# Performance work log

Hardware: AMD Instinct MI355X
Metric: run time of the kernel (lower is better)

Reference implementation:

```python
import jax, jax.numpy as jnp
import numpy as np

EMB = 256   # EMB_SIZE hard-coded in source
H = 8       # num heads (all heads share the same Q/K/V, as in source)
DK = EMB // H  # 32
B, T = 16, 2048
LN_EPS = 1e-5


def _layernorm(a, g, b):
    m = jnp.mean(a, axis=-1, keepdims=True)
    v = jnp.mean(jnp.square(a - m), axis=-1, keepdims=True)
    return (a - m) * jax.lax.rsqrt(v + LN_EPS) * g + b


def setup_inputs() -> dict:
    key = jax.random.key(0)
    ks = jax.random.split(key, 8)
    sc = 0.02
    return {
        "x": jax.random.normal(ks[0], (B, T, EMB), jnp.float32),
        "Wq": jax.random.normal(ks[1], (EMB, DK), jnp.float32) * sc,
        "Wk": jax.random.normal(ks[2], (EMB, DK), jnp.float32) * sc,
        "Wv": jax.random.normal(ks[3], (EMB, DK), jnp.float32) * sc,
        "Wp": jax.random.normal(ks[4], (EMB, EMB), jnp.float32) * sc,
        "bp": jnp.zeros((EMB,), jnp.float32),
        "W1": jax.random.normal(ks[5], (EMB, 4 * EMB), jnp.float32) * sc,
        "b1": jnp.zeros((4 * EMB,), jnp.float32),
        "W2": jax.random.normal(ks[6], (4 * EMB, EMB), jnp.float32) * sc,
        "b2": jnp.zeros((EMB,), jnp.float32),
        "g1": jnp.ones((EMB,), jnp.float32),
        "be1": jnp.zeros((EMB,), jnp.float32),
        "g2": jnp.ones((EMB,), jnp.float32),
        "be2": jnp.zeros((EMB,), jnp.float32),
    }


def reference(x, Wq, Wk, Wv, Wp, bp, W1, b1, W2, b2, g1, be1, g2, be2):
    # Single shared-head QKV projections (bias-free), as in source
    q = x @ Wq  # [B,T,DK]
    k = x @ Wk
    v = x @ Wv
    # Causal self-attention with explicit score matrix [B,T,T]
    scores = jnp.einsum("btd,bsd->bts", q, k) / jnp.sqrt(jnp.float32(DK))
    causal = jnp.tril(jnp.ones((T, T), dtype=bool))
    scores = jnp.where(causal, scores, -jnp.inf)
    a = jax.nn.softmax(scores, axis=-1)
    attn = jnp.einsum("bts,bsd->btd", a, v)  # [B,T,DK]
    # Source concatenates h identical copies of the same attention output
    cat = jnp.tile(attn, (1, 1, H))  # [B,T,EMB]
    mh = cat @ Wp + bp
    y1 = _layernorm(x + mh, g1, be1)
    ff = jax.nn.gelu(y1 @ W1 + b1, approximate=False) @ W2 + b2
    return _layernorm(y1 + ff, g2, be2)
```

## Files before the change

### kernel.cpp

```cpp
#include <hip/hip_runtime.h>

#define BB 16
#define TT 2048
#define EE 256
#define DK 32
#define MM (BB*TT)
#define FF 1024

typedef __bf16 bf16_t;
typedef __bf16 bf16x8 __attribute__((ext_vector_type(8)));
typedef __bf16 bf16x4 __attribute__((ext_vector_type(4)));
typedef float  f32x4  __attribute__((ext_vector_type(4)));

__device__ __forceinline__ f32x4 mfma16(bf16x8 a, bf16x8 b, f32x4 c){
  return __builtin_amdgcn_mfma_f32_16x16x32_bf16(a, b, c, 0, 0, 0);
}
__device__ __forceinline__ void gload_lds16(const void* g, void* l){
  __builtin_amdgcn_global_load_lds((__attribute__((address_space(1))) void*)g,
                                   (__attribute__((address_space(3))) void*)l,
                                   16, 0, 0);
}

__launch_bounds__(256)
__global__ void prep_kernel(const float* __restrict__ Wq, const float* __restrict__ Wk,
                            const float* __restrict__ Wv, const float* __restrict__ Wp,
                            const float* __restrict__ W1, const float* __restrict__ W2,
                            bf16_t* __restrict__ wqkv, float* __restrict__ wpe,
                            bf16_t* __restrict__ w1t, bf16_t* __restrict__ w2t)
{
  const int i = blockIdx.x*256 + threadIdx.x;
  if (i < 96*256) {
    const int r = i >> 8, c = i & 255;
    float v;
    if (r < 32)      v = Wq[c*32 + r] * 0.17677669529663687f;
    else if (r < 64) v = Wk[c*32 + (r-32)];
    else             v = Wv[c*32 + (r-64)];
    wqkv[i] = (bf16_t)v;
  }
  if (i < 32*256) {
    const int d = i >> 8, n = i & 255;
    float s = 0.f;
    #pragma unroll
    for (int h = 0; h < 8; ++h) s += Wp[(h*32 + d)*256 + n];
    wpe[i] = s;
  }
  if (i < 1024*256) {
    const int n = i >> 8, k = i & 255;
    w1t[i] = (bf16_t)W1[(size_t)k*1024 + n];
  }
  if (i < 256*1024) {
    const int n = i >> 10, k = i & 1023;
    w2t[i] = (bf16_t)W2[(size_t)k*256 + n];
  }
}

__launch_bounds__(256)
__global__ void qkv_kernel(const float* __restrict__ x, const bf16_t* __restrict__ wqkv,
                           bf16_t* __restrict__ q, bf16_t* __restrict__ kd,
                           bf16_t* __restrict__ vT)
{
  __shared__ bf16_t Ws[96*256];
  bf16_t* Vt = Ws;
  const int tid = threadIdx.x;
  #pragma unroll
  for (int i = 0; i < 12; ++i) {
    const int v8  = tid + i*256;
    const int row = v8 >> 5;
    const int bir = (v8 & 31) * 16;
    *(bf16x8*)((char*)Ws + row*512 + (bir ^ ((row & 7) << 4))) =
        *(const bf16x8*)(wqkv + (size_t)v8*8);
  }
  __syncthreads();

  const int w = tid >> 6, l = tid & 63;
  const int lr = l & 15, lk4 = l >> 4, lkb = lk4*8;
  const int m0 = blockIdx.x * 64;
  const int arow = m0 + w*16 + lr;
  const float* xr = x + (size_t)arow * 256;

  f32x4 acc[6] = {};
  #pragma unroll
  for (int s = 0; s < 8; ++s) {
    const int kb = s*32 + lkb;
    const float4 v0 = *(const float4*)(xr + kb);
    const float4 v1 = *(const float4*)(xr + kb + 4);
    bf16x8 a;
    a[0]=(bf16_t)v0.x; a[1]=(bf16_t)v0.y; a[2]=(bf16_t)v0.z; a[3]=(bf16_t)v0.w;
    a[4]=(bf16_t)v1.x; a[5]=(bf16_t)v1.y; a[6]=(bf16_t)v1.z; a[7]=(bf16_t)v1.w;
    #pragma unroll
    for (int j = 0; j < 6; ++j) {
      const int nrow = j*16 + lr;
      const bf16x8 bf = *(const bf16x8*)((const char*)Ws + nrow*512 +
                                         ((kb*2) ^ ((nrow & 7) << 4)));
      acc[j] = mfma16(a, bf, acc[j]);
    }
  }
  #pragma unroll
  for (int j = 0; j < 4; ++j) {
    #pragma unroll
    for (int r = 0; r < 4; ++r) {
      const int orow = m0 + w*16 + lk4*4 + r;
      const int col  = j*16 + lr;
      const bf16_t v = (bf16_t)acc[j][r];
      if (col < 32) q[(size_t)orow*32 + col] = v;
      else          kd[(size_t)orow*32 + (col-32)] = v;
    }
  }
  __syncthreads();
  #pragma unroll
  for (int j = 4; j < 6; ++j)
    #pragma unroll
    for (int r = 0; r < 4; ++r) {
      const int d = (j-4)*16 + lr;
      const int t = w*16 + lk4*4 + r;
      *(bf16_t*)((char*)Vt + d*128 + ((((t>>3) ^ (d&7))<<4) | ((t&7)*2))) =
          (bf16_t)acc[j][r];
    }
  __syncthreads();
  {
    const int d = tid >> 3, c8 = tid & 7;
    const bf16x8 v = *(const bf16x8*)((char*)Vt + d*128 + ((c8 ^ (d&7))<<4));
    *(bf16x8*)(vT + ((size_t)(m0 >> 11)*32 + d)*TT + (m0 & 2047) + c8*8) = v;
  }
}

__launch_bounds__(256)
__global__ void attnp_kernel(const bf16_t* __restrict__ q, const bf16_t* __restrict__ kd,
                             const bf16_t* __restrict__ vT,
                             float* __restrict__ part_acc, float* __restrict__ part_ml)
{
  __shared__ bf16_t P[4][16*128];
  const int tid = threadIdx.x;
  const int w = tid >> 6, l = tid & 63;
  const int wv = blockIdx.x*4 + w;
  const int lr = l & 15, g4 = l >> 4;
  const float NEG_INF = -__builtin_inff();

  const int b = wv / 320;
  const int u = wv - b*320;
  int r, base;
  if      (u >= 192) { r = 3; base = 192; }
  else if (u >= 96)  { r = 2; base = 96;  }
  else if (u >= 32)  { r = 1; base = 32;  }
  else               { r = 0; base = 0;   }
  const int qq = u - base;
  const int g  = r*32 + qq / (r+1);
  const int c  = qq - (qq / (r+1))*(r+1);
  const int t_total = (g >> 3) + 1;
  const int t0 = c*4;
  const int t1 = min(t0 + 4, t_total);

  const bf16_t* qb = q  + (size_t)b*TT*32;
  const bf16_t* kb = kd + (size_t)b*TT*32;
  const bf16_t* vb = vT + (size_t)b*32*TT;
  const int q0 = g*16;
  const int qg = q0 + lr;

  const bf16x8 qa = *(const bf16x8*)(qb + (size_t)(q0 + lr)*32 + g4*8);
  const bf16_t* v0r = vb + (size_t)lr*TT;
  const bf16_t* v1r = vb + (size_t)(16 + lr)*TT;

  f32x4 acc0 = {0.f,0.f,0.f,0.f}, acc1 = {0.f,0.f,0.f,0.f};
  float mrun = NEG_INF, lsum = 0.f;
  char* pb = (char*)&P[w][0];
  const int swz = (lr & 7) << 4;
  const f32x4 zf = {0.f,0.f,0.f,0.f};

  for (int t = t0; t < t1; ++t) {
    const int k0 = t * 128;
    f32x4 s[8];
    #pragma unroll
    for (int cc = 0; cc < 8; ++cc) {
      const bf16x8 kf = *(const bf16x8*)(kb + (size_t)(k0 + cc*16 + lr)*32 + g4*8);
      s[cc] = mfma16(kf, qa, zf);
    }
    if (t == t_total - 1) {
      #pragma unroll
      for (int cc = 0; cc < 8; ++cc)
        #pragma unroll
        for (int rr = 0; rr < 4; ++rr)
          if (k0 + cc*16 + g4*4 + rr > qg) s[cc][rr] = NEG_INF;
    }
    float mt = NEG_INF;
    #pragma unroll
    for (int cc = 0; cc < 8; ++cc) {
      float a01 = fmaxf(s[cc][0], s[cc][1]), a23 = fmaxf(s[cc][2], s[cc][3]);
      mt = fmaxf(mt, fmaxf(a01, a23));
    }
    mt = fmaxf(mt, __shfl_xor(mt, 16));
    mt = fmaxf(mt, __shfl_xor(mt, 32));
    const float mn = fmaxf(mrun, mt);
    const float sc = __expf(mrun - mn);
    float ps = 0.f;
    #pragma unroll
    for (int cc = 0; cc < 8; ++cc) {
      float p0 = __expf(s[cc][0]-mn), p1 = __expf(s[cc][1]-mn);
      float p2 = __expf(s[cc][2]-mn), p3 = __expf(s[cc][3]-mn);
      s[cc][0]=p0; s[cc][1]=p1; s[cc][2]=p2; s[cc][3]=p3;
      ps += (p0+p1) + (p2+p3);
    }
    ps += __shfl_xor(ps, 16);
    ps += __shfl_xor(ps, 32);
    lsum = lsum*sc + ps;
    mrun = mn;
    acc0 *= sc; acc1 *= sc;
    #pragma unroll
    for (int cc = 0; cc < 8; ++cc) {
      bf16x4 pk;
      pk[0]=(bf16_t)s[cc][0]; pk[1]=(bf16_t)s[cc][1];
      pk[2]=(bf16_t)s[cc][2]; pk[3]=(bf16_t)s[cc][3];
      *(bf16x4*)(pb + lr*256 + ((cc*32 + g4*8) ^ swz)) = pk;
    }
    #pragma unroll
    for (int h = 0; h < 4; ++h) {
      const bf16x8 pbf = *(const bf16x8*)(pb + lr*256 + ((h*64 + g4*16) ^ swz));
      acc0 = mfma16(*(const bf16x8*)(v0r + k0 + h*32 + g4*8), pbf, acc0);
      acc1 = mfma16(*(const bf16x8*)(v1r + k0 + h*32 + g4*8), pbf, acc1);
    }
  }
  float* pa = part_acc + (size_t)wv*512;
  *(f32x4*)(pa + l*8)     = acc0;
  *(f32x4*)(pa + l*8 + 4) = acc1;
  if (l < 16) {
    part_ml[wv*32 + l]      = mrun;
    part_ml[wv*32 + 16 + l] = lsum;
  }
}

__launch_bounds__(256)
__global__ void attnc_kernel(const float* __restrict__ part_acc,
                             const float* __restrict__ part_ml,
                             bf16_t* __restrict__ attn)
{
  const int tid = threadIdx.x;
  const int id = blockIdx.x*4 + (tid >> 6);
  const int l = tid & 63, lr = l & 15, g4 = l >> 4;
  const int b = id >> 7, g = id & 127;
  const int r = g >> 5;
  const int base = (r == 0) ? 0 : (r == 1) ? 32 : (r == 2) ? 96 : 192;
  const int p0 = b*320 + base + (g - (r << 5))*(r + 1);
  const int nc = r + 1;
  const float NEG_INF = -__builtin_inff();

  float m0v=NEG_INF,m1v=NEG_INF,m2v=NEG_INF,m3v=NEG_INF;
  float l0v=0,l1v=0,l2v=0,l3v=0;
  f32x4 a00={0,0,0,0},a01={0,0,0,0},a10={0,0,0,0},a11={0,0,0,0};
  f32x4 a20={0,0,0,0},a21={0,0,0,0},a30={0,0,0,0},a31={0,0,0,0};
  {
    const float* pa = part_acc + (size_t)p0*512;
    a00 = *(const f32x4*)(pa + l*8); a01 = *(const f32x4*)(pa + l*8 + 4);
    m0v = part_ml[p0*32 + lr]; l0v = part_ml[p0*32 + 16 + lr];
  }
  if (nc > 1) {
    const float* pa = part_acc + (size_t)(p0+1)*512;
    a10 = *(const f32x4*)(pa + l*8); a11 = *(const f32x4*)(pa + l*8 + 4);
    m1v = part_ml[(p0+1)*32 + lr]; l1v = part_ml[(p0+1)*32 + 16 + lr];
  }
  if (nc > 2) {
    const float* pa = part_acc + (size_t)(p0+2)*512;
    a20 = *(const f32x4*)(pa + l*8); a21 = *(const f32x4*)(pa + l*8 + 4);
    m2v = part_ml[(p0+2)*32 + lr]; l2v = part_ml[(p0+2)*32 + 16 + lr];
  }
  if (nc > 3) {
    const float* pa = part_acc + (size_t)(p0+3)*512;
    a30 = *(const f32x4*)(pa + l*8); a31 = *(const f32x4*)(pa + l*8 + 4);
    m3v = part_ml[(p0+3)*32 + lr]; l3v = part_ml[(p0+3)*32 + 16 + lr];
  }
  const float M = fmaxf(fmaxf(m0v, m1v), fmaxf(m2v, m3v));
  const float w0 = __expf(m0v - M), w1 = __expf(m1v - M);
  const float w2 = __expf(m2v - M), w3 = __expf(m3v - M);
  const float L = l0v*w0 + l1v*w1 + l2v*w2 + l3v*w3;
  const float inv = 1.0f / L;
  f32x4 o0 = (a00*w0 + a10*w1 + a20*w2 + a30*w3) * inv;
  f32x4 o1 = (a01*w0 + a11*w1 + a21*w2 + a31*w3) * inv;

  bf16_t* ao = attn + ((size_t)b*TT + g*16 + lr)*32;
  bf16x4 ob0, ob1;
  ob0[0]=(bf16_t)o0[0]; ob0[1]=(bf16_t)o0[1]; ob0[2]=(bf16_t)o0[2]; ob0[3]=(bf16_t)o0[3];
  ob1[0]=(bf16_t)o1[0]; ob1[1]=(bf16_t)o1[1]; ob1[2]=(bf16_t)o1[2]; ob1[3]=(bf16_t)o1[3];
  *(bf16x4*)(ao + g4*4)      = ob0;
  *(bf16x4*)(ao + 16 + g4*4) = ob1;
}

__launch_bounds__(256)
__global__ void ln1_kernel(const float* __restrict__ x, const bf16_t* __restrict__ attn,
                           const float* __restrict__ wpe, const float* __restrict__ bp,
                           const float* __restrict__ g1, const float* __restrict__ be1,
                           bf16_t* __restrict__ y1b)
{
  __shared__ float Wp_s[32*256];
  const int tid = threadIdx.x;
  for (int i = tid; i < 32*64; i += 256)
    ((float4*)Wp_s)[i] = ((const float4*)wpe)[i];
  __syncthreads();

  const int w = tid >> 6, l = tid & 63;
  const int n = l * 4;
  const float4 gv  = *(const float4*)(g1  + n);
  const float4 bev = *(const float4*)(be1 + n);
  const float4 bpv = *(const float4*)(bp  + n);

  #pragma unroll 1
  for (int it = 0; it < 8; ++it) {
    const int row = blockIdx.x*32 + it*4 + w;
    const bf16_t* ar = attn + (size_t)row*32;
    float a[32];
    #pragma unroll
    for (int i = 0; i < 4; ++i) {
      const bf16x8 t = *(const bf16x8*)(ar + i*8);
      #pragma unroll
      for (int j = 0; j < 8; ++j) a[i*8 + j] = (float)t[j];
    }
    float mh[4] = {bpv.x, bpv.y, bpv.z, bpv.w};
    #pragma unroll
    for (int d = 0; d < 32; ++d) {
      const float4 wv = *(const float4*)(Wp_s + d*256 + n);
      const float ad = a[d];
      mh[0] = fmaf(ad, wv.x, mh[0]); mh[1] = fmaf(ad, wv.y, mh[1]);
      mh[2] = fmaf(ad, wv.z, mh[2]); mh[3] = fmaf(ad, wv.w, mh[3]);
    }
    const float4 xv = *(const float4*)(x + (size_t)row*256 + n);
    const float t0 = xv.x + mh[0], t1 = xv.y + mh[1];
    const float t2 = xv.z + mh[2], t3 = xv.w + mh[3];
    float s1 = (t0+t1) + (t2+t3);
    float s2 = (t0*t0 + t1*t1) + (t2*t2 + t3*t3);
    #pragma unroll
    for (int m = 1; m < 64; m <<= 1) { s1 += __shfl_xor(s1, m); s2 += __shfl_xor(s2, m); }
    const float mean = s1 * (1.0f/256.0f);
    const float var  = s2 * (1.0f/256.0f) - mean*mean;
    const float rs   = rsqrtf(var + 1e-5f);
    float4 yv;
    yv.x = (t0-mean)*rs*gv.x + bev.x; yv.y = (t1-mean)*rs*gv.y + bev.y;
    yv.z = (t2-mean)*rs*gv.z + bev.z; yv.w = (t3-mean)*rs*gv.w + bev.w;
    bf16x4 yb; yb[0]=(bf16_t)yv.x; yb[1]=(bf16_t)yv.y; yb[2]=(bf16_t)yv.z; yb[3]=(bf16_t)yv.w;
    *(bf16x4*)(y1b + (size_t)row*256 + n) = yb;
  }
}

__launch_bounds__(512)
__global__ void mlp_kernel(const bf16_t* __restrict__ y1b, const bf16_t* __restrict__ w1t,
                           const float* __restrict__ b1, const bf16_t* __restrict__ w2t,
                           const float* __restrict__ b2, const float* __restrict__ g2,
                           const float* __restrict__ be2, float* __restrict__ out)
{
  __shared__ char SM[151552];
  const int tid = threadIdx.x;
  const int w = tid >> 6, l = tid & 63;
  const int lr = l & 15, lk4 = l >> 4;
  const int m0 = blockIdx.x * 128;
  const int wm1 = (w>>1)*32, wn1 = (w&1)*32;
  const int wm2 = (w>>2)*64, wn2 = (w&3)*64;

  {
    const float2 bv = *(const float2*)(b1 + tid*2);
    *(float2*)(SM + 147456 + tid*8) = bv;
  }
  asm volatile("s_waitcnt vmcnt(0) lgkmcnt(0)" ::: "memory");
  __builtin_amdgcn_sched_barrier(0);

  #define ST_W1(i, d)                                                         \
    { _Pragma("unroll")                                                       \
      for (int p_ = 0; p_ < 4; ++p_) {                                        \
        const int idx_ = p_*512 + tid;                                        \
        const int r_ = idx_ >> 5, c_ = idx_ & 31;                             \
        const int sc_ = (c_ & 24) | ((c_ ^ r_) & 7);                          \
        gload_lds16(w1t + (size_t)((i)*64 + r_)*256 + sc_*8,                  \
                    SM + (d)*32768 + idx_*16);                                \
      } }
  #define ST_W2(i, d)                                                         \
    { _Pragma("unroll")                                                       \
      for (int p_ = 0; p_ < 4; ++p_) {                                        \
        const int idx_ = p_*512 + tid;                                        \
        const int r_ = idx_ >> 3, c_ = idx_ & 7;                              \
        gload_lds16(w2t + (size_t)r_*1024 + (i)*64 + ((c_ ^ r_) & 7)*8,       \
                    SM + 65536 + (d)*32768 + idx_*16);                        \
      } }

  ST_W1(0, 0);
  __builtin_amdgcn_sched_barrier(0);
  bf16x8 aA[2][8];
  #pragma unroll
  for (int i2 = 0; i2 < 2; ++i2)
    #pragma unroll
    for (int kk = 0; kk < 8; ++kk)
      aA[i2][kk] = *(const bf16x8*)(y1b +
          (size_t)(m0 + wm1 + i2*16 + lr)*256 + kk*32 + lk4*8);
  __builtin_amdgcn_sched_barrier(0);
  ST_W2(0, 0);
  __builtin_amdgcn_sched_barrier(0);
  ST_W1(1, 1);
  __builtin_amdgcn_sched_barrier(0);

  f32x4 oacc[4][4] = {};

  #pragma unroll 1
  for (int i = 0; i < 16; ++i) {
    if (i < 15) { asm volatile("s_waitcnt vmcnt(8)" ::: "memory"); }
    else        { asm volatile("s_waitcnt vmcnt(4)" ::: "memory"); }
    __builtin_amdgcn_sched_barrier(0);
    __builtin_amdgcn_s_barrier();
    __builtin_amdgcn_sched_barrier(0);
    const char* sw1 = SM + (i & 1)*32768;
    f32x4 ah[2][2] = {};
    __builtin_amdgcn_s_setprio(1);
    #pragma unroll
    for (int kk = 0; kk < 8; ++kk) {
      const int off = kk*64 + lk4*16;
      const int n0r = wn1 + lr, n1r = wn1 + 16 + lr;
      const bf16x8 bf0 = *(const bf16x8*)(sw1 + n0r*512 + (off ^ ((n0r&7)<<4)));
      const bf16x8 bf1 = *(const bf16x8*)(sw1 + n1r*512 + (off ^ ((n1r&7)<<4)));
      ah[0][0] = mfma16(aA[0][kk], bf0, ah[0][0]);
      ah[0][1] = mfma16(aA[0][kk], bf1, ah[0][1]);
      ah[1][0] = mfma16(aA[1][kk], bf0, ah[1][0]);
      ah[1][1] = mfma16(aA[1][kk], bf1, ah[1][1]);
    }
    __builtin_amdgcn_s_setprio(0);
    #pragma unroll
    for (int j = 0; j < 2; ++j) {
      const float bias = *(const float*)(SM + 147456 + (i*64 + wn1 + j*16 + lr)*4);
      #pragma unroll
      for (int i2 = 0; i2 < 2; ++i2)
        #pragma unroll
        for (int r = 0; r < 4; ++r) {
          const int hrow = wm1 + i2*16 + lk4*4 + r;
          const int hcol = wn1 + j*16 + lr;
          const float v = ah[i2][j][r] + bias;
          const float z = 1.5957691216057308f * v * fmaf(0.044715f, v*v, 1.0f);
          const float gg = v * __builtin_amdgcn_rcpf(1.0f + __expf(-z));
          *(bf16_t*)(SM + 131072 + hrow*128 + ((hcol*2) ^ ((hrow&7)<<4))) = (bf16_t)gg;
        }
    }
    asm volatile("s_waitcnt lgkmcnt(0)" ::: "memory");
    __builtin_amdgcn_sched_barrier(0);
    if (i < 15) { asm volatile("s_waitcnt vmcnt(4)" ::: "memory"); }
    else        { asm volatile("s_waitcnt vmcnt(0)" ::: "memory"); }
    __builtin_amdgcn_sched_barrier(0);
    __builtin_amdgcn_s_barrier();
    __builtin_amdgcn_sched_barrier(0);
    const char* sw2 = SM + 65536 + (i & 1)*32768;
    __builtin_amdgcn_s_setprio(1);
    #pragma unroll
    for (int kk2 = 0; kk2 < 2; ++kk2) {
      const int off = kk2*64 + lk4*16;
      bf16x8 ha[4], wb[4];
      #pragma unroll
      for (int i3 = 0; i3 < 4; ++i3) {
        const int row = wm2 + i3*16 + lr;
        ha[i3] = *(const bf16x8*)(SM + 131072 + row*128 + (off ^ ((row&7)<<4)));
      }
      #pragma unroll
      for (int j3 = 0; j3 < 4; ++j3) {
        const int n = wn2 + j3*16 + lr;
        wb[j3] = *(const bf16x8*)(sw2 + n*128 + (off ^ ((n&7)<<4)));
      }
      #pragma unroll
      for (int i3 = 0; i3 < 4; ++i3)
        #pragma unroll
        for (int j3 = 0; j3 < 4; ++j3)
          oacc[i3][j3] = mfma16(ha[i3], wb[j3], oacc[i3][j3]);
    }
    __builtin_amdgcn_s_setprio(0);
    __builtin_amdgcn_sched_barrier(0);
    if (i < 15) { ST_W2(i+1, (i+1)&1); }
    __builtin_amdgcn_sched_barrier(0);
    if (i < 14) { ST_W1(i+2, i&1); }
    __builtin_amdgcn_sched_barrier(0);
  }
  #undef ST_W1
  #undef ST_W2

  float b2r[4], g2r[4], be2r[4];
  #pragma unroll
  for (int j3 = 0; j3 < 4; ++j3) {
    const int col = wn2 + j3*16 + lr;
    b2r[j3] = b2[col]; g2r[j3] = g2[col]; be2r[j3] = be2[col];
  }
  #pragma unroll
  for (int i3 = 0; i3 < 4; ++i3)
    #pragma unroll
    for (int r = 0; r < 4; ++r) {
      const int grow = m0 + wm2 + i3*16 + lk4*4 + r;
      #pragma unroll
      for (int j3 = 0; j3 < 4; ++j3) {
        const int col = wn2 + j3*16 + lr;
        oacc[i3][j3][r] += b2r[j3] + (float)y1b[(size_t)grow*256 + col];
      }
    }
  __syncthreads();
  float* red = (float*)SM;
  #pragma unroll
  for (int i3 = 0; i3 < 4; ++i3)
    #pragma unroll
    for (int r = 0; r < 4; ++r) {
      float s1 = (oacc[i3][0][r] + oacc[i3][1][r]) + (oacc[i3][2][r] + oacc[i3][3][r]);
      float s2 = (oacc[i3][0][r]*oacc[i3][0][r] + oacc[i3][1][r]*oacc[i3][1][r]) +
                 (oacc[i3][2][r]*oacc[i3][2][r] + oacc[i3][3][r]*oacc[i3][3][r]);
      #pragma unroll
      for (int m = 1; m < 16; m <<= 1) { s1 += __shfl_xor(s1, m); s2 += __shfl_xor(s2, m); }
      if (lr == 0) {
        const int rl = wm2 + i3*16 + lk4*4 + r;
        red[rl*8 + (w & 3)*2]     = s1;
        red[rl*8 + (w & 3)*2 + 1] = s2;
      }
    }
  __syncthreads();
  #pragma unroll
  for (int i3 = 0; i3 < 4; ++i3)
    #pragma unroll
    for (int r = 0; r < 4; ++r) {
      const int rl = wm2 + i3*16 + lk4*4 + r;
      const float S1 = (red[rl*8+0] + red[rl*8+2]) + (red[rl*8+4] + red[rl*8+6]);
      const float S2 = (red[rl*8+1] + red[rl*8+3]) + (red[rl*8+5] + red[rl*8+7]);
      const float mean = S1 * (1.0f/256.0f);
      const float var  = S2 * (1.0f/256.0f) - mean*mean;
      const float rs   = rsqrtf(var + 1e-5f);
      #pragma unroll
      for (int j3 = 0; j3 < 4; ++j3) {
        const int col = wn2 + j3*16 + lr;
        out[(size_t)(m0 + rl)*256 + col] = (oacc[i3][j3][r] - mean)*rs*g2r[j3] + be2r[j3];
      }
    }
}

extern "C" void kernel_launch(void* const* d_in, const int* in_sizes, int n_in,
                              void* d_out, int out_size, void* d_ws, size_t ws_size,
                              hipStream_t stream)
{
  const float* x   = (const float*)d_in[0];
  const float* Wq  = (const float*)d_in[1];
  const float* Wk  = (const float*)d_in[2];
  const float* Wv  = (const float*)d_in[3];
  const float* Wp  = (const float*)d_in[4];
  const float* bp  = (const float*)d_in[5];
  const float* W1  = (const float*)d_in[6];
  const float* b1  = (const float*)d_in[7];
  const float* W2  = (const float*)d_in[8];
  const float* b2  = (const float*)d_in[9];
  const float* g1  = (const float*)d_in[10];
  const float* be1 = (const float*)d_in[11];
  const float* g2  = (const float*)d_in[12];
  const float* be2 = (const float*)d_in[13];

  char* ws = (char*)d_ws;
  bf16_t* qd   = (bf16_t*)(ws + ((size_t)0  << 20));
  bf16_t* kd   = (bf16_t*)(ws + ((size_t)2  << 20));
  bf16_t* vTd  = (bf16_t*)(ws + ((size_t)4  << 20));
  bf16_t* attn = (bf16_t*)(ws + ((size_t)6  << 20));
  bf16_t* y1b  = (bf16_t*)(ws + ((size_t)8  << 20));
  bf16_t* wqkv = (bf16_t*)(ws + ((size_t)24 << 20));
  float*  wpe  = (float*) (ws + ((size_t)25 << 20));
  bf16_t* w1t  = (bf16_t*)(ws + ((size_t)26 << 20));
  bf16_t* w2t  = (bf16_t*)(ws + ((size_t)27 << 20));
  float*  pml  = (float*) (ws + ((size_t)28 << 20));
  float*  pacc = (float*) (ws + ((size_t)29 << 20));
  float* out = (float*)d_out;

  prep_kernel<<<1024, 256, 0, stream>>>(Wq, Wk, Wv, Wp, W1, W2, wqkv, wpe, w1t, w2t);
  qkv_kernel<<<512, 256, 0, stream>>>(x, wqkv, qd, kd, vTd);
  attnp_kernel<<<1280, 256, 0, stream>>>(qd, kd, vTd, pacc, pml);
  attnc_kernel<<<512, 256, 0, stream>>>(pacc, pml, attn);
  ln1_kernel<<<1024, 256, 0, stream>>>(x, attn, wpe, bp, g1, be1, y1b);
  mlp_kernel<<<256, 512, 0, stream>>>(y1b, w1t, b1, w2t, b2, g2, be2, out);
}
```

Baseline: 129.7 us.

## Double MLP block to 1024 threads with per-wave 16-row tiles

The fused MLP kernel now launches 16 waves per block instead of 8, and each wave owns a 16-row by 32-col slice of the hidden GEMM and a 16-row by 128-col slice of the output GEMM. Cooperative weight staging and the LayerNorm reduction are re-indexed for the wider block, with fewer loads per thread and matching vmcnt waits. Some sched_barrier fences are removed. The aim is more latency hiding per CU for the same LDS footprint, at the cost of less register-level reuse per MFMA, more LDS reads per flop, and a tighter register budget per thread.

```diff
diff --git a/kernel.cpp b/kernel.cpp
--- a/kernel.cpp
+++ b/kernel.cpp
@@ -337,7 +337,7 @@
   }
 }
 
-__launch_bounds__(512)
+__launch_bounds__(1024)
 __global__ void mlp_kernel(const bf16_t* __restrict__ y1b, const bf16_t* __restrict__ w1t,
                            const float* __restrict__ b1, const bf16_t* __restrict__ w2t,
                            const float* __restrict__ b2, const float* __restrict__ g2,
@@ -346,22 +346,20 @@
   __shared__ char SM[151552];
   const int tid = threadIdx.x;
   const int w = tid >> 6, l = tid & 63;
-  const int lr = l & 15, lk4 = l >> 4;
+  const int lr = l & 15, g4 = l >> 4;
   const int m0 = blockIdx.x * 128;
-  const int wm1 = (w>>1)*32, wn1 = (w&1)*32;
-  const int wm2 = (w>>2)*64, wn2 = (w&3)*64;
-
-  {
-    const float2 bv = *(const float2*)(b1 + tid*2);
-    *(float2*)(SM + 147456 + tid*8) = bv;
-  }
+  const int wm  = (w >> 1) * 16;
+  const int wn1 = (w & 1) * 32;
+  const int wn2 = (w & 1) * 128;
+
+  *(float*)(SM + 147456 + tid*4) = b1[tid];
   asm volatile("s_waitcnt vmcnt(0) lgkmcnt(0)" ::: "memory");
   __builtin_amdgcn_sched_barrier(0);
 
   #define ST_W1(i, d)                                                         \
     { _Pragma("unroll")                                                       \
-      for (int p_ = 0; p_ < 4; ++p_) {                                        \
-        const int idx_ = p_*512 + tid;                                        \
+      for (int p_ = 0; p_ < 2; ++p_) {                                        \
+        const int idx_ = p_*1024 + tid;                                       \
         const int r_ = idx_ >> 5, c_ = idx_ & 31;                             \
         const int sc_ = (c_ & 24) | ((c_ ^ r_) & 7);                          \
         gload_lds16(w1t + (size_t)((i)*64 + r_)*256 + sc_*8,                  \
@@ -369,157 +367,129 @@
       } }
   #define ST_W2(i, d)                                                         \
     { _Pragma("unroll")                                                       \
-      for (int p_ = 0; p_ < 4; ++p_) {                                        \
-        const int idx_ = p_*512 + tid;                                        \
+      for (int p_ = 0; p_ < 2; ++p_) {                                        \
+        const int idx_ = p_*1024 + tid;                                       \
         const int r_ = idx_ >> 3, c_ = idx_ & 7;                              \
         gload_lds16(w2t + (size_t)r_*1024 + (i)*64 + ((c_ ^ r_) & 7)*8,       \
                     SM + 65536 + (d)*32768 + idx_*16);                        \
       } }
 
   ST_W1(0, 0);
-  __builtin_amdgcn_sched_barrier(0);
-  bf16x8 aA[2][8];
-  #pragma unroll
-  for (int i2 = 0; i2 < 2; ++i2)
-    #pragma unroll
-    for (int kk = 0; kk < 8; ++kk)
-      aA[i2][kk] = *(const bf16x8*)(y1b +
-          (size_t)(m0 + wm1 + i2*16 + lr)*256 + kk*32 + lk4*8);
-  __builtin_amdgcn_sched_barrier(0);
+  bf16x8 aA[8];
+  #pragma unroll
+  for (int kk = 0; kk < 8; ++kk)
+    aA[kk] = *(const bf16x8*)(y1b + (size_t)(m0 + wm + lr)*256 + kk*32 + g4*8);
   ST_W2(0, 0);
-  __builtin_amdgcn_sched_barrier(0);
   ST_W1(1, 1);
-  __builtin_amdgcn_sched_barrier(0);
-
-  f32x4 oacc[4][4] = {};
+
+  f32x4 oacc[8] = {};
+  char* hb = SM + 131072;
 
   #pragma unroll 1
   for (int i = 0; i < 16; ++i) {
-    if (i < 15) { asm volatile("s_waitcnt vmcnt(8)" ::: "memory"); }
-    else        { asm volatile("s_waitcnt vmcnt(4)" ::: "memory"); }
+    if (i < 15) { asm volatile("s_waitcnt vmcnt(4)" ::: "memory"); }
+    else        { asm volatile("s_waitcnt vmcnt(2)" ::: "memory"); }
     __builtin_amdgcn_sched_barrier(0);
     __builtin_amdgcn_s_barrier();
-    __builtin_amdgcn_sched_barrier(0);
     const char* sw1 = SM + (i & 1)*32768;
-    f32x4 ah[2][2] = {};
+    f32x4 ah0 = {0.f,0.f,0.f,0.f}, ah1 = {0.f,0.f,0.f,0.f};
     __builtin_amdgcn_s_setprio(1);
     #pragma unroll
     for (int kk = 0; kk < 8; ++kk) {
-      const int off = kk*64 + lk4*16;
+      const int off = kk*64 + g4*16;
       const int n0r = wn1 + lr, n1r = wn1 + 16 + lr;
-      const bf16x8 bf0 = *(const bf16x8*)(sw1 + n0r*512 + (off ^ ((n0r&7)<<4)));
-      const bf16x8 bf1 = *(const bf16x8*)(sw1 + n1r*512 + (off ^ ((n1r&7)<<4)));
-      ah[0][0] = mfma16(aA[0][kk], bf0, ah[0][0]);
-      ah[0][1] = mfma16(aA[0][kk], bf1, ah[0][1]);
-      ah[1][0] = mfma16(aA[1][kk], bf0, ah[1][0]);
-      ah[1][1] = mfma16(aA[1][kk], bf1, ah[1][1]);
+      const bf16x8 bf0 = *(const bf16x8*)(sw1 + n0r*512 + (off ^ ((n0r & 7) << 4)));
+      const bf16x8 bf1 = *(const bf16x8*)(sw1 + n1r*512 + (off ^ ((n1r & 7) << 4)));
+      ah0 = mfma16(aA[kk], bf0, ah0);
+      ah1 = mfma16(aA[kk], bf1, ah1);
     }
     __builtin_amdgcn_s_setprio(0);
     #pragma unroll
     for (int j = 0; j < 2; ++j) {
       const float bias = *(const float*)(SM + 147456 + (i*64 + wn1 + j*16 + lr)*4);
+      const f32x4 av = j ? ah1 : ah0;
+      const int hcol2 = (wn1 + j*16 + lr)*2;
       #pragma unroll
-      for (int i2 = 0; i2 < 2; ++i2)
-        #pragma unroll
-        for (int r = 0; r < 4; ++r) {
-          const int hrow = wm1 + i2*16 + lk4*4 + r;
-          const int hcol = wn1 + j*16 + lr;
-          const float v = ah[i2][j][r] + bias;
-          const float z = 1.5957691216057308f * v * fmaf(0.044715f, v*v, 1.0f);
-          const float gg = v * __builtin_amdgcn_rcpf(1.0f + __expf(-z));
-          *(bf16_t*)(SM + 131072 + hrow*128 + ((hcol*2) ^ ((hrow&7)<<4))) = (bf16_t)gg;
-        }
+      for (int r = 0; r < 4; ++r) {
+        const int hrow = wm + g4*4 + r;
+        const float v = av[r] + bias;
+        const float z = 1.5957691216057308f * v * fmaf(0.044715f, v*v, 1.0f);
+        const float gg = v * __builtin_amdgcn_rcpf(1.0f + __expf(-z));
+        *(bf16_t*)(hb + hrow*128 + (hcol2 ^ ((hrow & 7) << 4))) = (bf16_t)gg;
+      }
     }
     asm volatile("s_waitcnt lgkmcnt(0)" ::: "memory");
     __builtin_amdgcn_sched_barrier(0);
-    if (i < 15) { asm volatile("s_waitcnt vmcnt(4)" ::: "memory"); }
+    if (i < 15) { asm volatile("s_waitcnt vmcnt(2)" ::: "memory"); }
     else        { asm volatile("s_waitcnt vmcnt(0)" ::: "memory"); }
     __builtin_amdgcn_sched_barrier(0);
     __builtin_amdgcn_s_barrier();
-    __builtin_amdgcn_sched_barrier(0);
     const char* sw2 = SM + 65536 + (i & 1)*32768;
     __builtin_amdgcn_s_setprio(1);
     #pragma unroll
     for (int kk2 = 0; kk2 < 2; ++kk2) {
-      const int off = kk2*64 + lk4*16;
-      bf16x8 ha[4], wb[4];
+      const int off = kk2*64 + g4*16;
+      const int hr = wm + lr;
+      const bf16x8 ha = *(const bf16x8*)(hb + hr*128 + (off ^ ((hr & 7) << 4)));
       #pragma unroll
-      for (int i3 = 0; i3 < 4; ++i3) {
-        const int row = wm2 + i3*16 + lr;
-        ha[i3] = *(const bf16x8*)(SM + 131072 + row*128 + (off ^ ((row&7)<<4)));
+      for (int j3 = 0; j3 < 8; ++j3) {
+        const int n = wn2 + j3*16 + lr;
+        const bf16x8 wb = *(const bf16x8*)(sw2 + n*128 + (off ^ ((n & 7) << 4)));
+        oacc[j3] = mfma16(ha, wb, oacc[j3]);
       }
-      #pragma unroll
-      for (int j3 = 0; j3 < 4; ++j3) {
-        const int n = wn2 + j3*16 + lr;
-        wb[j3] = *(const bf16x8*)(sw2 + n*128 + (off ^ ((n&7)<<4)));
-      }
-      #pragma unroll
-      for (int i3 = 0; i3 < 4; ++i3)
-        #pragma unroll
-        for (int j3 = 0; j3 < 4; ++j3)
-          oacc[i3][j3] = mfma16(ha[i3], wb[j3], oacc[i3][j3]);
     }
     __builtin_amdgcn_s_setprio(0);
-    __builtin_amdgcn_sched_barrier(0);
-    if (i < 15) { ST_W2(i+1, (i+1)&1); }
-    __builtin_amdgcn_sched_barrier(0);
-    if (i < 14) { ST_W1(i+2, i&1); }
-    __builtin_amdgcn_sched_barrier(0);
+    if (i < 15) ST_W2(i+1, (i+1)&1);
+    if (i < 14) ST_W1(i+2, i&1);
   }
   #undef ST_W1
   #undef ST_W2
 
-  float b2r[4], g2r[4], be2r[4];
-  #pragma unroll
-  for (int j3 = 0; j3 < 4; ++j3) {
+  float b2r[8], g2r[8], be2r[8];
+  #pragma unroll
+  for (int j3 = 0; j3 < 8; ++j3) {
     const int col = wn2 + j3*16 + lr;
     b2r[j3] = b2[col]; g2r[j3] = g2[col]; be2r[j3] = be2[col];
   }
   #pragma unroll
-  for (int i3 = 0; i3 < 4; ++i3)
-    #pragma unroll
-    for (int r = 0; r < 4; ++r) {
-      const int grow = m0 + wm2 + i3*16 + lk4*4 + r;
-      #pragma unroll
-      for (int j3 = 0; j3 < 4; ++j3) {
-        const int col = wn2 + j3*16 + lr;
-        oacc[i3][j3][r] += b2r[j3] + (float)y1b[(size_t)grow*256 + col];
-      }
-    }
+  for (int r = 0; r < 4; ++r) {
+    const int grow = m0 + wm + g4*4 + r;
+    #pragma unroll
+    for (int j3 = 0; j3 < 8; ++j3) {
+      const int col = wn2 + j3*16 + lr;
+      oacc[j3][r] += b2r[j3] + (float)y1b[(size_t)grow*256 + col];
+    }
+  }
   __syncthreads();
   float* red = (float*)SM;
   #pragma unroll
-  for (int i3 = 0; i3 < 4; ++i3)
-    #pragma unroll
-    for (int r = 0; r < 4; ++r) {
-      float s1 = (oacc[i3][0][r] + oacc[i3][1][r]) + (oacc[i3][2][r] + oacc[i3][3][r]);
-      float s2 = (oacc[i3][0][r]*oacc[i3][0][r] + oacc[i3][1][r]*oacc[i3][1][r]) +
-                 (oacc[i3][2][r]*oacc[i3][2][r] + oacc[i3][3][r]*oacc[i3][3][r]);
-      #pragma unroll
-      for (int m = 1; m < 16; m <<= 1) { s1 += __shfl_xor(s1, m); s2 += __shfl_xor(s2, m); }
-      if (lr == 0) {
-        const int rl = wm2 + i3*16 + lk4*4 + r;
-        red[rl*8 + (w & 3)*2]     = s1;
-        red[rl*8 + (w & 3)*2 + 1] = s2;
-      }
-    }
+  for (int r = 0; r < 4; ++r) {
+    float s1 = 0.f, s2 = 0.f;
+    #pragma unroll
+    for (int j3 = 0; j3 < 8; ++j3) { s1 += oacc[j3][r]; s2 += oacc[j3][r]*oacc[j3][r]; }
+    #pragma unroll
+    for (int m = 1; m < 16; m <<= 1) { s1 += __shfl_xor(s1, m); s2 += __shfl_xor(s2, m); }
+    if (lr == 0) {
+      const int rl = wm + g4*4 + r;
+      red[rl*4 + (w & 1)*2]     = s1;
+      red[rl*4 + (w & 1)*2 + 1] = s2;
+    }
+  }
   __syncthreads();
   #pragma unroll
-  for (int i3 = 0; i3 < 4; ++i3)
-    #pragma unroll
-    for (int r = 0; r < 4; ++r) {
-      const int rl = wm2 + i3*16 + lk4*4 + r;
-      const float S1 = (red[rl*8+0] + red[rl*8+2]) + (red[rl*8+4] + red[rl*8+6]);
-      const float S2 = (red[rl*8+1] + red[rl*8+3]) + (red[rl*8+5] + red[rl*8+7]);
-      const float mean = S1 * (1.0f/256.0f);
-      const float var  = S2 * (1.0f/256.0f) - mean*mean;
-      const float rs   = rsqrtf(var + 1e-5f);
-      #pragma unroll
-      for (int j3 = 0; j3 < 4; ++j3) {
-        const int col = wn2 + j3*16 + lr;
-        out[(size_t)(m0 + rl)*256 + col] = (oacc[i3][j3][r] - mean)*rs*g2r[j3] + be2r[j3];
-      }
-    }
+  for (int r = 0; r < 4; ++r) {
+    const int rl = wm + g4*4 + r;
+    const float S1 = red[rl*4+0] + red[rl*4+2];
+    const float S2 = red[rl*4+1] + red[rl*4+3];
+    const float mean = S1 * (1.0f/256.0f);
+    const float var  = S2 * (1.0f/256.0f) - mean*mean;
+    const float rs   = rsqrtf(var + 1e-5f);
+    #pragma unroll
+    for (int j3 = 0; j3 < 8; ++j3) {
+      const int col = wn2 + j3*16 + lr;
+      out[(size_t)(m0 + rl)*256 + col] = (oacc[j3][r] - mean)*rs*g2r[j3] + be2r[j3];
+    }
+  }
 }
 
 extern "C" void kernel_launch(void* const* d_in, const int* in_sizes, int n_in,
@@ -560,5 +530,5 @@
   attnp_kernel<<<1280, 256, 0, stream>>>(qd, kd, vTd, pacc, pml);
   attnc_kernel<<<512, 256, 0, stream>>>(pacc, pml, attn);
   ln1_kernel<<<1024, 256, 0, stream>>>(x, attn, wpe, bp, g1, be1, y1b);
-  mlp_kernel<<<256, 512, 0, stream>>>(y1b, w1t, b1, w2t, b2, g2, be2, out);
-}
+  mlp_kernel<<<256, 1024, 0, stream>>>(y1b, w1t, b1, w2t, b2, g2, be2, out);
+}
```

Measured after the change: 132.9 us. +2.4%, slower.
